# Kernel tuning notes

Hardware: AMD Instinct MI355X
Metric: run time of the kernel (lower is better)

## Reference

```python
import jax, jax.numpy as jnp
import numpy as np

L = 44                      # num_lods
IMG = 178                   # output image side
HASH_SIZE = 1 << 10         # codebook_bitwidth = 10
PRIME = np.uint32(2654435761)
RES = np.round(16.0 * (128.0 / 16.0) ** (np.arange(L) / (L - 1.0))).astype(np.int32)
DENSE = (RES + 1) ** 2 <= HASH_SIZE            # dense level if it fits in 2^10 entries
SIZES = np.where(DENSE, (RES + 1) ** 2, HASH_SIZE).astype(np.int32)
OFFS = np.concatenate([[0], np.cumsum(SIZES)[:-1]]).astype(np.int32)
TOTAL = int(SIZES.sum())    # 38584 shared codebook entries (latent_dim = 1)


def setup_inputs() -> dict:
    key = jax.random.key(0)
    k = jax.random.split(key, 5)
    B, N = 16, IMG * IMG
    x = jax.random.uniform(k[0], (B, N, 2), dtype=jnp.float32)            # 2D coords in [0,1]
    codebook = 0.1 * jax.random.normal(k[1], (B, TOTAL, 1), jnp.float32)  # feature_std=0.1
    w1 = jax.random.normal(k[2], (B, 16, L), jnp.float32) / np.sqrt(L)
    w2 = jax.random.normal(k[3], (B, 16, 16), jnp.float32) / 4.0
    w3 = jax.random.normal(k[4], (B, 3, 16), jnp.float32) / 4.0
    return {"x": x, "codebook": codebook, "w1": w1, "w2": w2, "w3": w3}


def _grid_lookup(x, codebook):
    """Multi-LOD hashed 2D grid bilinear lookup. x:[B,N,2], codebook:[B,T,1] -> [B,N,L]."""
    B, N, _ = x.shape
    res_f = jnp.asarray(RES, jnp.float32)
    res_i = jnp.asarray(RES)
    scaled = x[:, :, None, :] * res_f[None, None, :, None]          # [B,N,L,2]
    base = jnp.floor(scaled)
    frac = scaled - base
    base = base.astype(jnp.int32)
    corners = jnp.array([[0, 0], [0, 1], [1, 0], [1, 1]], jnp.int32)  # [4,2]
    c = base[:, :, :, None, :] + corners[None, None, None]          # [B,N,L,4,2]
    c = jnp.minimum(c, res_i[None, None, :, None, None])
    cx, cy = c[..., 0], c[..., 1]
    dense_idx = cy * (res_i + 1)[None, None, :, None] + cx          # row-major dense index
    h = (cx.astype(jnp.uint32) ^ (cy.astype(jnp.uint32) * PRIME)) % jnp.uint32(HASH_SIZE)
    idx = jnp.where(jnp.asarray(DENSE)[None, None, :, None], dense_idx, h.astype(jnp.int32))
    idx = idx + jnp.asarray(OFFS)[None, None, :, None]              # [B,N,L,4] into shared table
    vals = jnp.take_along_axis(codebook[:, :, 0], idx.reshape(B, -1), axis=1).reshape(B, N, L, 4)
    fr = frac[:, :, :, None, :]                                     # [B,N,L,1,2]
    w = jnp.where(corners[None, None, None] == 1, fr, 1.0 - fr).prod(-1)  # bilinear wts [B,N,L,4]
    return (vals * w).sum(-1)                                       # [B,N,L]


def reference(x, codebook, w1, w2, w3):
    feats = _grid_lookup(x, codebook)                               # [B,N,44] ('cat' multiscale)
    h = jax.nn.relu(jnp.einsum('bnl,bhl->bnh', feats, w1))          # per-sample hypernet weights
    h = jax.nn.relu(jnp.einsum('bnh,bkh->bnk', h, w2))
    rgb = jax.nn.sigmoid(jnp.einsum('bnk,bck->bnc', h, w3))         # [B,N,3]
    return rgb.reshape(x.shape[0], IMG, IMG, 3)
```

## Files before the change

### kernel.cpp

```cpp
#include <hip/hip_runtime.h>
#include <math.h>

#define NLEV 44
#define NDENSE 15
#define IMG 178
#define NPTS (IMG*IMG)
#define HASH_SIZE 1024
#define PRIME 2654435761u
#define BLOCK 1024
#define PTS_PER_BLOCK (2*BLOCK)

typedef __attribute__((ext_vector_type(2))) float f32x2;

struct LevelParams {
    int res[NLEV];
    int offs[NLEV];
    int total;
};

#define PKFMA_S(acc, a, b) \
    asm("v_pk_fma_f32 %0, %1, %2, %0" : "+v"(acc) : "v"(a), "s"(b))

__global__ __launch_bounds__(1024) void transpose_w1(const float* __restrict__ w1,
                                                     float* __restrict__ w1t) {
    const int b = blockIdx.x;
    const int i = threadIdx.x;
    if (i < 16 * NLEV) {
        const int l = i >> 4, o = i & 15;
        w1t[(size_t)b * 16 * NLEV + i] = w1[(size_t)b * 16 * NLEV + o * NLEV + l];
    }
}

template<bool TP>
__global__ __launch_bounds__(BLOCK) void shacira_kernel(
    const float* __restrict__ x, const float* __restrict__ codebook,
    const float* __restrict__ w1, const float* __restrict__ w1t,
    const float* __restrict__ w2, const float* __restrict__ w3,
    float* __restrict__ out, LevelParams lp)
{
    extern __shared__ float sCB[];
    const int total = lp.total;
    const int tid = threadIdx.x;
    const int b = blockIdx.y;

    {
        const float* cbg = codebook + (size_t)b * total;
        const float4* src = (const float4*)cbg;
        float4* dst = (float4*)sCB;
        const int n4 = total >> 2;
        for (int i = tid; i < n4; i += BLOCK) dst[i] = src[i];
        for (int i = (n4 << 2) + tid; i < total; i += BLOCK) sCB[i] = cbg[i];
    }
    __syncthreads();

    const float* w1b = TP ? (w1t + (size_t)b * 16 * NLEV) : (w1 + (size_t)b * 16 * NLEV);
    const float* w2b = w2 + (size_t)b * 256;
    const float* w3b = w3 + (size_t)b * 48;

    const int n0 = blockIdx.x * PTS_PER_BLOCK + tid;
    const int n1 = n0 + BLOCK;
    const bool valid0 = n0 < NPTS;
    const bool valid1 = n1 < NPTS;
    const float2* xg = (const float2*)x + (size_t)b * NPTS;
    float2 xy0 = valid0 ? xg[n0] : make_float2(0.f, 0.f);
    float2 xy1 = valid1 ? xg[n1] : make_float2(0.f, 0.f);

    f32x2 h1a[8], h1b[8];
#pragma unroll
    for (int j = 0; j < 8; ++j) {
        h1a[j].x = 0.f; h1a[j].y = 0.f;
        h1b[j].x = 0.f; h1b[j].y = 0.f;
    }

#pragma unroll
    for (int l = 0; l < NDENSE; ++l) {
        const int res = lp.res[l];
        const int st  = res + 1;
        const int off = lp.offs[l];
        const float rf = (float)res;
        f32x2 wlv[8];
        if constexpr (TP) {
            const f32x2* wp = (const f32x2*)(w1b + l * 16);
#pragma unroll
            for (int j = 0; j < 8; ++j) wlv[j] = wp[j];
        } else {
#pragma unroll
            for (int j = 0; j < 8; ++j) {
                wlv[j].x = w1b[(2 * j) * NLEV + l];
                wlv[j].y = w1b[(2 * j + 1) * NLEV + l];
            }
        }
        auto dolevel = [&](const float2 xy, f32x2* h1) {
            const float sx = xy.x * rf, sy = xy.y * rf;
            const int ix0 = (int)sx, iy0 = (int)sy;
            const float fx = sx - (float)ix0, fy = sy - (float)iy0;
            const int r0 = off + iy0 * st + ix0;
            const float v00 = sCB[r0],      v10 = sCB[r0 + 1];
            const float v01 = sCB[r0 + st], v11 = sCB[r0 + st + 1];
            const float vx0 = fmaf(fx, v10 - v00, v00);
            const float vx1 = fmaf(fx, v11 - v01, v01);
            const float feat = fmaf(fy, vx1 - vx0, vx0);
            f32x2 f2; f2.x = feat; f2.y = feat;
#pragma unroll
            for (int j = 0; j < 8; ++j) PKFMA_S(h1[j], f2, wlv[j]);
        };
        dolevel(xy0, h1a);
        dolevel(xy1, h1b);
    }

#pragma unroll
    for (int l = NDENSE; l < NLEV; ++l) {
        const int res = lp.res[l];
        const int off = lp.offs[l];
        const float rf = (float)res;
        f32x2 wlv[8];
        if constexpr (TP) {
            const f32x2* wp = (const f32x2*)(w1b + l * 16);
#pragma unroll
            for (int j = 0; j < 8; ++j) wlv[j] = wp[j];
        } else {
#pragma unroll
            for (int j = 0; j < 8; ++j) {
                wlv[j].x = w1b[(2 * j) * NLEV + l];
                wlv[j].y = w1b[(2 * j + 1) * NLEV + l];
            }
        }
        auto dolevel = [&](const float2 xy, f32x2* h1) {
            const float sx = xy.x * rf, sy = xy.y * rf;
            const int ix0 = (int)sx, iy0 = (int)sy;
            const float fx = sx - (float)ix0, fy = sy - (float)iy0;
            const unsigned px0 = (unsigned)ix0, px1 = px0 + 1u;
            const unsigned py0 = (unsigned)iy0 * PRIME, py1 = py0 + PRIME;
            const int i00 = (int)((px0 ^ py0) & (HASH_SIZE - 1));
            const int i01 = (int)((px0 ^ py1) & (HASH_SIZE - 1));
            const int i10 = (int)((px1 ^ py0) & (HASH_SIZE - 1));
            const int i11 = (int)((px1 ^ py1) & (HASH_SIZE - 1));
            const float v00 = sCB[off + i00];
            const float v01 = sCB[off + i01];
            const float v10 = sCB[off + i10];
            const float v11 = sCB[off + i11];
            const float vx0 = fmaf(fx, v10 - v00, v00);
            const float vx1 = fmaf(fx, v11 - v01, v01);
            const float feat = fmaf(fy, vx1 - vx0, vx0);
            f32x2 f2; f2.x = feat; f2.y = feat;
#pragma unroll
            for (int j = 0; j < 8; ++j) PKFMA_S(h1[j], f2, wlv[j]);
        };
        dolevel(xy0, h1a);
        dolevel(xy1, h1b);
    }

    auto mlp = [&](f32x2* h1, int n, bool valid) {
        if (!valid) return;
#pragma unroll
        for (int j = 0; j < 8; ++j) {
            h1[j].x = fmaxf(h1[j].x, 0.f);
            h1[j].y = fmaxf(h1[j].y, 0.f);
        }
        float h2[16];
#pragma unroll
        for (int o = 0; o < 16; ++o) {
            const f32x2* w2v = (const f32x2*)(w2b + o * 16);
            f32x2 acc; acc.x = 0.f; acc.y = 0.f;
#pragma unroll
            for (int k = 0; k < 8; ++k) PKFMA_S(acc, h1[k], w2v[k]);
            h2[o] = fmaxf(acc.x + acc.y, 0.f);
        }
        f32x2 h2v[8];
#pragma unroll
        for (int j = 0; j < 8; ++j) { h2v[j].x = h2[2 * j]; h2v[j].y = h2[2 * j + 1]; }
        float rgb[3];
#pragma unroll
        for (int c = 0; c < 3; ++c) {
            const f32x2* w3v = (const f32x2*)(w3b + c * 16);
            f32x2 acc; acc.x = 0.f; acc.y = 0.f;
#pragma unroll
            for (int k = 0; k < 8; ++k) PKFMA_S(acc, h2v[k], w3v[k]);
            rgb[c] = 1.f / (1.f + expf(-(acc.x + acc.y)));
        }
        float* op = out + ((size_t)b * NPTS + n) * 3;
        op[0] = rgb[0]; op[1] = rgb[1]; op[2] = rgb[2];
    };
    mlp(h1a, n0, valid0);
    mlp(h1b, n1, valid1);
}

extern "C" void kernel_launch(void* const* d_in, const int* in_sizes, int n_in,
                              void* d_out, int out_size, void* d_ws, size_t ws_size,
                              hipStream_t stream) {
    const float* x        = (const float*)d_in[0];
    const float* codebook = (const float*)d_in[1];
    const float* w1       = (const float*)d_in[2];
    const float* w2       = (const float*)d_in[3];
    const float* w3       = (const float*)d_in[4];
    float* out = (float*)d_out;

    const int B = in_sizes[0] / (NPTS * 2);

    LevelParams lp;
    int off = 0;
    for (int l = 0; l < NLEV; ++l) {
        const double r = 16.0 * pow(128.0 / 16.0, (double)l / (double)(NLEV - 1));
        const int res = (int)llrint(r);
        lp.res[l] = res;
        lp.offs[l] = off;
        const int sz = ((long long)(res + 1) * (res + 1) <= HASH_SIZE)
                           ? (res + 1) * (res + 1) : HASH_SIZE;
        off += sz;
    }
    lp.total = off;

    const size_t smemBytes = (size_t)lp.total * 4;
    const size_t w1tBytes = (size_t)B * 16 * NLEV * 4;
    const bool tp = ws_size >= w1tBytes;

    if (tp) {
        transpose_w1<<<dim3(B), dim3(1024), 0, stream>>>(w1, (float*)d_ws);
        hipFuncSetAttribute((const void*)shacira_kernel<true>,
                            hipFuncAttributeMaxDynamicSharedMemorySize, (int)smemBytes);
        dim3 grid((NPTS + PTS_PER_BLOCK - 1) / PTS_PER_BLOCK, B);
        shacira_kernel<true><<<grid, dim3(BLOCK), smemBytes, stream>>>(
            x, codebook, w1, (const float*)d_ws, w2, w3, out, lp);
    } else {
        hipFuncSetAttribute((const void*)shacira_kernel<false>,
                            hipFuncAttributeMaxDynamicSharedMemorySize, (int)smemBytes);
        dim3 grid((NPTS + PTS_PER_BLOCK - 1) / PTS_PER_BLOCK, B);
        shacira_kernel<false><<<grid, dim3(BLOCK), smemBytes, stream>>>(
            x, codebook, w1, (const float*)0, w2, w3, out, lp);
    }
}
```

Measured before the change: 39.51 us.

## Stage only hash levels in LDS as fp16, read dense levels from global

```diff
diff --git a/kernel.cpp b/kernel.cpp
--- a/kernel.cpp
+++ b/kernel.cpp
@@ -1,14 +1,15 @@
 #include <hip/hip_runtime.h>
+#include <hip/hip_fp16.h>
 #include <math.h>
 
 #define NLEV 44
 #define NDENSE 15
+#define NHASH (NLEV - NDENSE)
 #define IMG 178
 #define NPTS (IMG*IMG)
 #define HASH_SIZE 1024
 #define PRIME 2654435761u
 #define BLOCK 1024
-#define PTS_PER_BLOCK (2*BLOCK)
 
 typedef __attribute__((ext_vector_type(2))) float f32x2;
 
@@ -16,6 +17,7 @@
     int res[NLEV];
     int offs[NLEV];
     int total;
+    int hashBase;
 };
 
 #define PKFMA_S(acc, a, b) \
@@ -32,157 +34,156 @@
 }
 
 template<bool TP>
-__global__ __launch_bounds__(BLOCK) void shacira_kernel(
+__device__ __forceinline__ void load_w1(const float* __restrict__ w1b, int l, f32x2* wlv) {
+    if constexpr (TP) {
+        const f32x2* wp = (const f32x2*)(w1b + l * 16);
+#pragma unroll
+        for (int j = 0; j < 8; ++j) wlv[j] = wp[j];
+    } else {
+#pragma unroll
+        for (int j = 0; j < 8; ++j) {
+            wlv[j].x = w1b[(2 * j) * NLEV + l];
+            wlv[j].y = w1b[(2 * j + 1) * NLEV + l];
+        }
+    }
+}
+
+template<int L0, int CNT, bool TP>
+__device__ __forceinline__ void dense_g(
+    const LevelParams& lp, const float* __restrict__ cbg,
+    const float* __restrict__ w1b, float2 xy, f32x2* __restrict__ h1)
+{
+    float v[CNT][4];
+    float fr[CNT][2];
+#pragma unroll
+    for (int i = 0; i < CNT; ++i) {
+        const int l = L0 + i;
+        const int res = lp.res[l];
+        const int st  = res + 1;
+        const int off = lp.offs[l];
+        const float rf = (float)res;
+        const float sx = xy.x * rf, sy = xy.y * rf;
+        const int ix0 = (int)sx, iy0 = (int)sy;
+        fr[i][0] = sx - (float)ix0;
+        fr[i][1] = sy - (float)iy0;
+        const int r0 = off + iy0 * st + ix0;
+        v[i][0] = cbg[r0];
+        v[i][1] = cbg[r0 + 1];
+        v[i][2] = cbg[r0 + st];
+        v[i][3] = cbg[r0 + st + 1];
+    }
+#pragma unroll
+    for (int i = 0; i < CNT; ++i) {
+        const int l = L0 + i;
+        f32x2 wlv[8];
+        load_w1<TP>(w1b, l, wlv);
+        const float vx0 = fmaf(fr[i][0], v[i][1] - v[i][0], v[i][0]);
+        const float vx1 = fmaf(fr[i][0], v[i][3] - v[i][2], v[i][2]);
+        const float feat = fmaf(fr[i][1], vx1 - vx0, vx0);
+        f32x2 f2; f2.x = feat; f2.y = feat;
+#pragma unroll
+        for (int j = 0; j < 8; ++j) PKFMA_S(h1[j], f2, wlv[j]);
+    }
+}
+
+template<bool TP>
+__global__ __launch_bounds__(BLOCK, 4) void shacira_kernel(
     const float* __restrict__ x, const float* __restrict__ codebook,
     const float* __restrict__ w1, const float* __restrict__ w1t,
     const float* __restrict__ w2, const float* __restrict__ w3,
     float* __restrict__ out, LevelParams lp)
 {
-    extern __shared__ float sCB[];
-    const int total = lp.total;
+    extern __shared__ __half sH[];
     const int tid = threadIdx.x;
     const int b = blockIdx.y;
+    const float* cbg = codebook + (size_t)b * lp.total;
 
     {
-        const float* cbg = codebook + (size_t)b * total;
-        const float4* src = (const float4*)cbg;
-        float4* dst = (float4*)sCB;
-        const int n4 = total >> 2;
-        for (int i = tid; i < n4; i += BLOCK) dst[i] = src[i];
-        for (int i = (n4 << 2) + tid; i < total; i += BLOCK) sCB[i] = cbg[i];
+        const float4* src = (const float4*)(cbg + lp.hashBase);
+        __half2* dst = (__half2*)sH;
+        const int n4 = (NHASH * HASH_SIZE) >> 2;
+        for (int i = tid; i < n4; i += BLOCK) {
+            const float4 v = src[i];
+            dst[2 * i]     = __floats2half2_rn(v.x, v.y);
+            dst[2 * i + 1] = __floats2half2_rn(v.z, v.w);
+        }
     }
     __syncthreads();
+
+    const int n = blockIdx.x * BLOCK + tid;
+    if (n >= NPTS) return;
 
     const float* w1b = TP ? (w1t + (size_t)b * 16 * NLEV) : (w1 + (size_t)b * 16 * NLEV);
     const float* w2b = w2 + (size_t)b * 256;
     const float* w3b = w3 + (size_t)b * 48;
 
-    const int n0 = blockIdx.x * PTS_PER_BLOCK + tid;
-    const int n1 = n0 + BLOCK;
-    const bool valid0 = n0 < NPTS;
-    const bool valid1 = n1 < NPTS;
-    const float2* xg = (const float2*)x + (size_t)b * NPTS;
-    float2 xy0 = valid0 ? xg[n0] : make_float2(0.f, 0.f);
-    float2 xy1 = valid1 ? xg[n1] : make_float2(0.f, 0.f);
-
-    f32x2 h1a[8], h1b[8];
+    const float2 xy = ((const float2*)x)[(size_t)b * NPTS + n];
+
+    f32x2 h1[8];
+#pragma unroll
+    for (int j = 0; j < 8; ++j) { h1[j].x = 0.f; h1[j].y = 0.f; }
+
+    dense_g<0, 3, TP>(lp, cbg, w1b, xy, h1);
+    dense_g<3, 3, TP>(lp, cbg, w1b, xy, h1);
+    dense_g<6, 3, TP>(lp, cbg, w1b, xy, h1);
+    dense_g<9, 3, TP>(lp, cbg, w1b, xy, h1);
+    dense_g<12, 3, TP>(lp, cbg, w1b, xy, h1);
+
+#pragma unroll
+    for (int l = NDENSE; l < NLEV; ++l) {
+        const float rf = (float)lp.res[l];
+        const int base = (l - NDENSE) << 10;
+        const float sx = xy.x * rf, sy = xy.y * rf;
+        const int ix0 = (int)sx, iy0 = (int)sy;
+        const float fx = sx - (float)ix0, fy = sy - (float)iy0;
+        const unsigned px0 = (unsigned)ix0, px1 = px0 + 1u;
+        const unsigned py0 = (unsigned)iy0 * PRIME, py1 = py0 + PRIME;
+        const int i00 = (int)((px0 ^ py0) & (HASH_SIZE - 1));
+        const int i01 = (int)((px0 ^ py1) & (HASH_SIZE - 1));
+        const int i10 = (int)((px1 ^ py0) & (HASH_SIZE - 1));
+        const int i11 = (int)((px1 ^ py1) & (HASH_SIZE - 1));
+        const float v00 = __half2float(sH[base + i00]);
+        const float v01 = __half2float(sH[base + i01]);
+        const float v10 = __half2float(sH[base + i10]);
+        const float v11 = __half2float(sH[base + i11]);
+        const float vx0 = fmaf(fx, v10 - v00, v00);
+        const float vx1 = fmaf(fx, v11 - v01, v01);
+        const float feat = fmaf(fy, vx1 - vx0, vx0);
+        f32x2 f2; f2.x = feat; f2.y = feat;
+        f32x2 wlv[8];
+        load_w1<TP>(w1b, l, wlv);
+#pragma unroll
+        for (int j = 0; j < 8; ++j) PKFMA_S(h1[j], f2, wlv[j]);
+    }
+
 #pragma unroll
     for (int j = 0; j < 8; ++j) {
-        h1a[j].x = 0.f; h1a[j].y = 0.f;
-        h1b[j].x = 0.f; h1b[j].y = 0.f;
-    }
-
-#pragma unroll
-    for (int l = 0; l < NDENSE; ++l) {
-        const int res = lp.res[l];
-        const int st  = res + 1;
-        const int off = lp.offs[l];
-        const float rf = (float)res;
-        f32x2 wlv[8];
-        if constexpr (TP) {
-            const f32x2* wp = (const f32x2*)(w1b + l * 16);
-#pragma unroll
-            for (int j = 0; j < 8; ++j) wlv[j] = wp[j];
-        } else {
-#pragma unroll
-            for (int j = 0; j < 8; ++j) {
-                wlv[j].x = w1b[(2 * j) * NLEV + l];
-                wlv[j].y = w1b[(2 * j + 1) * NLEV + l];
-            }
-        }
-        auto dolevel = [&](const float2 xy, f32x2* h1) {
-            const float sx = xy.x * rf, sy = xy.y * rf;
-            const int ix0 = (int)sx, iy0 = (int)sy;
-            const float fx = sx - (float)ix0, fy = sy - (float)iy0;
-            const int r0 = off + iy0 * st + ix0;
-            const float v00 = sCB[r0],      v10 = sCB[r0 + 1];
-            const float v01 = sCB[r0 + st], v11 = sCB[r0 + st + 1];
-            const float vx0 = fmaf(fx, v10 - v00, v00);
-            const float vx1 = fmaf(fx, v11 - v01, v01);
-            const float feat = fmaf(fy, vx1 - vx0, vx0);
-            f32x2 f2; f2.x = feat; f2.y = feat;
-#pragma unroll
-            for (int j = 0; j < 8; ++j) PKFMA_S(h1[j], f2, wlv[j]);
-        };
-        dolevel(xy0, h1a);
-        dolevel(xy1, h1b);
-    }
-
-#pragma unroll
-    for (int l = NDENSE; l < NLEV; ++l) {
-        const int res = lp.res[l];
-        const int off = lp.offs[l];
-        const float rf = (float)res;
-        f32x2 wlv[8];
-        if constexpr (TP) {
-            const f32x2* wp = (const f32x2*)(w1b + l * 16);
-#pragma unroll
-            for (int j = 0; j < 8; ++j) wlv[j] = wp[j];
-        } else {
-#pragma unroll
-            for (int j = 0; j < 8; ++j) {
-                wlv[j].x = w1b[(2 * j) * NLEV + l];
-                wlv[j].y = w1b[(2 * j + 1) * NLEV + l];
-            }
-        }
-        auto dolevel = [&](const float2 xy, f32x2* h1) {
-            const float sx = xy.x * rf, sy = xy.y * rf;
-            const int ix0 = (int)sx, iy0 = (int)sy;
-            const float fx = sx - (float)ix0, fy = sy - (float)iy0;
-            const unsigned px0 = (unsigned)ix0, px1 = px0 + 1u;
-            const unsigned py0 = (unsigned)iy0 * PRIME, py1 = py0 + PRIME;
-            const int i00 = (int)((px0 ^ py0) & (HASH_SIZE - 1));
-            const int i01 = (int)((px0 ^ py1) & (HASH_SIZE - 1));
-            const int i10 = (int)((px1 ^ py0) & (HASH_SIZE - 1));
-            const int i11 = (int)((px1 ^ py1) & (HASH_SIZE - 1));
-            const float v00 = sCB[off + i00];
-            const float v01 = sCB[off + i01];
-            const float v10 = sCB[off + i10];
-            const float v11 = sCB[off + i11];
-            const float vx0 = fmaf(fx, v10 - v00, v00);
-            const float vx1 = fmaf(fx, v11 - v01, v01);
-            const float feat = fmaf(fy, vx1 - vx0, vx0);
-            f32x2 f2; f2.x = feat; f2.y = feat;
-#pragma unroll
-            for (int j = 0; j < 8; ++j) PKFMA_S(h1[j], f2, wlv[j]);
-        };
-        dolevel(xy0, h1a);
-        dolevel(xy1, h1b);
-    }
-
-    auto mlp = [&](f32x2* h1, int n, bool valid) {
-        if (!valid) return;
-#pragma unroll
-        for (int j = 0; j < 8; ++j) {
-            h1[j].x = fmaxf(h1[j].x, 0.f);
-            h1[j].y = fmaxf(h1[j].y, 0.f);
-        }
-        float h2[16];
-#pragma unroll
-        for (int o = 0; o < 16; ++o) {
-            const f32x2* w2v = (const f32x2*)(w2b + o * 16);
-            f32x2 acc; acc.x = 0.f; acc.y = 0.f;
-#pragma unroll
-            for (int k = 0; k < 8; ++k) PKFMA_S(acc, h1[k], w2v[k]);
-            h2[o] = fmaxf(acc.x + acc.y, 0.f);
-        }
-        f32x2 h2v[8];
-#pragma unroll
-        for (int j = 0; j < 8; ++j) { h2v[j].x = h2[2 * j]; h2v[j].y = h2[2 * j + 1]; }
-        float rgb[3];
-#pragma unroll
-        for (int c = 0; c < 3; ++c) {
-            const f32x2* w3v = (const f32x2*)(w3b + c * 16);
-            f32x2 acc; acc.x = 0.f; acc.y = 0.f;
-#pragma unroll
-            for (int k = 0; k < 8; ++k) PKFMA_S(acc, h2v[k], w3v[k]);
-            rgb[c] = 1.f / (1.f + expf(-(acc.x + acc.y)));
-        }
-        float* op = out + ((size_t)b * NPTS + n) * 3;
-        op[0] = rgb[0]; op[1] = rgb[1]; op[2] = rgb[2];
-    };
-    mlp(h1a, n0, valid0);
-    mlp(h1b, n1, valid1);
+        h1[j].x = fmaxf(h1[j].x, 0.f);
+        h1[j].y = fmaxf(h1[j].y, 0.f);
+    }
+    float h2[16];
+#pragma unroll
+    for (int o = 0; o < 16; ++o) {
+        const f32x2* w2v = (const f32x2*)(w2b + o * 16);
+        f32x2 acc; acc.x = 0.f; acc.y = 0.f;
+#pragma unroll
+        for (int k = 0; k < 8; ++k) PKFMA_S(acc, h1[k], w2v[k]);
+        h2[o] = fmaxf(acc.x + acc.y, 0.f);
+    }
+    f32x2 h2v[8];
+#pragma unroll
+    for (int j = 0; j < 8; ++j) { h2v[j].x = h2[2 * j]; h2v[j].y = h2[2 * j + 1]; }
+    float rgb[3];
+#pragma unroll
+    for (int c = 0; c < 3; ++c) {
+        const f32x2* w3v = (const f32x2*)(w3b + c * 16);
+        f32x2 acc; acc.x = 0.f; acc.y = 0.f;
+#pragma unroll
+        for (int k = 0; k < 8; ++k) PKFMA_S(acc, h2v[k], w3v[k]);
+        rgb[c] = 1.f / (1.f + expf(-(acc.x + acc.y)));
+    }
+    float* op = out + ((size_t)b * NPTS + n) * 3;
+    op[0] = rgb[0]; op[1] = rgb[1]; op[2] = rgb[2];
 }
 
 extern "C" void kernel_launch(void* const* d_in, const int* in_sizes, int n_in,
@@ -209,22 +210,18 @@
         off += sz;
     }
     lp.total = off;
-
-    const size_t smemBytes = (size_t)lp.total * 4;
+    lp.hashBase = lp.offs[NDENSE];
+
+    const size_t smemBytes = (size_t)NHASH * HASH_SIZE * sizeof(__half);
     const size_t w1tBytes = (size_t)B * 16 * NLEV * 4;
     const bool tp = ws_size >= w1tBytes;
 
+    dim3 grid((NPTS + BLOCK - 1) / BLOCK, B);
     if (tp) {
         transpose_w1<<<dim3(B), dim3(1024), 0, stream>>>(w1, (float*)d_ws);
-        hipFuncSetAttribute((const void*)shacira_kernel<true>,
-                            hipFuncAttributeMaxDynamicSharedMemorySize, (int)smemBytes);
-        dim3 grid((NPTS + PTS_PER_BLOCK - 1) / PTS_PER_BLOCK, B);
         shacira_kernel<true><<<grid, dim3(BLOCK), smemBytes, stream>>>(
             x, codebook, w1, (const float*)d_ws, w2, w3, out, lp);
     } else {
-        hipFuncSetAttribute((const void*)shacira_kernel<false>,
-                            hipFuncAttributeMaxDynamicSharedMemorySize, (int)smemBytes);
-        dim3 grid((NPTS + PTS_PER_BLOCK - 1) / PTS_PER_BLOCK, B);
         shacira_kernel<false><<<grid, dim3(BLOCK), smemBytes, stream>>>(
             x, codebook, w1, (const float*)0, w2, w3, out, lp);
     }
```

Measured after the change: 42.12 us. 6.6% more time.

## Specialize kernel with compile-time level constants and 4KB-aligned hash table layout

Applied to the files above, without the earlier changes.

```diff
diff --git a/kernel.cpp b/kernel.cpp
--- a/kernel.cpp
+++ b/kernel.cpp
@@ -3,14 +3,24 @@
 
 #define NLEV 44
 #define NDENSE 15
+#define NHASH (NLEV - NDENSE)
 #define IMG 178
 #define NPTS (IMG*IMG)
 #define HASH_SIZE 1024
 #define PRIME 2654435761u
 #define BLOCK 1024
 #define PTS_PER_BLOCK (2*BLOCK)
+#define HBASE 36864u
+#define PRIME_LOW_B 1732u
+#define PYMASK 4092u
 
 typedef __attribute__((ext_vector_type(2))) float f32x2;
+
+constexpr int RES_C[NLEV] = {16,17,18,18,19,20,21,22,24,25,26,27,29,30,31,
+                             33,35,36,38,40,42,44,46,49,51,54,56,59,62,65,
+                             68,72,75,79,83,87,91,96,101,105,111,116,122,128};
+constexpr int size_c(int l) { int r = RES_C[l]; int s = (r+1)*(r+1); return s <= 1024 ? s : 1024; }
+constexpr int off_c(int l)  { int o = 0; for (int i = 0; i < l; ++i) o += size_c(i); return o; }
 
 struct LevelParams {
     int res[NLEV];
@@ -20,6 +30,8 @@
 
 #define PKFMA_S(acc, a, b) \
     asm("v_pk_fma_f32 %0, %1, %2, %0" : "+v"(acc) : "v"(a), "s"(b))
+
+#define FRACT(dst, src) asm("v_fract_f32 %0, %1" : "=v"(dst) : "v"(src))
 
 __global__ __launch_bounds__(1024) void transpose_w1(const float* __restrict__ w1,
                                                      float* __restrict__ w1t) {
@@ -31,8 +43,171 @@
     }
 }
 
+
+template<int L>
+__device__ __forceinline__ float dense_feat(const char* lds, float2 xy) {
+    constexpr float rf = (float)RES_C[L];
+    constexpr int st = RES_C[L] + 1;
+    constexpr unsigned off4 = (unsigned)(off_c(L) * 4);
+    const float sx = xy.x * rf, sy = xy.y * rf;
+    const int ix0 = (int)sx, iy0 = (int)sy;
+    float fx, fy;
+    FRACT(fx, sx);
+    FRACT(fy, sy);
+    const unsigned aD = off4 + (((unsigned)(iy0 * st + ix0)) << 2);
+    const float v00 = *(const float*)(lds + aD);
+    const float v10 = *(const float*)(lds + aD + 4);
+    const float v01 = *(const float*)(lds + aD + 4 * st);
+    const float v11 = *(const float*)(lds + aD + 4 * st + 4);
+    const float vx0 = fmaf(fx, v10 - v00, v00);
+    const float vx1 = fmaf(fx, v11 - v01, v01);
+    return fmaf(fy, vx1 - vx0, vx0);
+}
+
+template<int L>
+__device__ __forceinline__ float hash_feat(const char* lds, float2 xy) {
+    constexpr float rf = (float)RES_C[L];
+    constexpr unsigned lbase = HBASE + (unsigned)(L - NDENSE) * 4096u;
+    const float sx = xy.x * rf, sy = xy.y * rf;
+    const int ix0 = (int)sx, iy0 = (int)sy;
+    float fx, fy;
+    FRACT(fx, sx);
+    FRACT(fy, sy);
+    const unsigned pyb0 = ((unsigned)iy0 * PRIME_LOW_B) & PYMASK;
+    const unsigned pyb1 = (pyb0 + PRIME_LOW_B) & PYMASK;
+    const unsigned bpx0 = lbase + (((unsigned)ix0) << 2);
+    const unsigned bpx1 = bpx0 + 4u;
+    const float v00 = *(const float*)(lds + (bpx0 ^ pyb0));
+    const float v01 = *(const float*)(lds + (bpx0 ^ pyb1));
+    const float v10 = *(const float*)(lds + (bpx1 ^ pyb0));
+    const float v11 = *(const float*)(lds + (bpx1 ^ pyb1));
+    const float vx0 = fmaf(fx, v10 - v00, v00);
+    const float vx1 = fmaf(fx, v11 - v01, v01);
+    return fmaf(fy, vx1 - vx0, vx0);
+}
+
+template<int L>
+__device__ __forceinline__ void level_apply(const float* __restrict__ w1b,
+                                            float f0, float f1,
+                                            f32x2* __restrict__ h1a, f32x2* __restrict__ h1b) {
+    const f32x2* wp = (const f32x2*)(w1b + L * 16);
+    f32x2 wlv[8];
+#pragma unroll
+    for (int j = 0; j < 8; ++j) wlv[j] = wp[j];
+    f32x2 f0v; f0v.x = f0; f0v.y = f0;
+    f32x2 f1v; f1v.x = f1; f1v.y = f1;
+#pragma unroll
+    for (int j = 0; j < 8; ++j) {
+        PKFMA_S(h1a[j], f0v, wlv[j]);
+        PKFMA_S(h1b[j], f1v, wlv[j]);
+    }
+}
+
+template<int L>
+__device__ __forceinline__ void levels_from(const char* lds, const float* __restrict__ w1b,
+                                            const float2& xy0, const float2& xy1,
+                                            f32x2* __restrict__ h1a, f32x2* __restrict__ h1b) {
+    if constexpr (L < NLEV) {
+        float f0, f1;
+        if constexpr (L < NDENSE) {
+            f0 = dense_feat<L>(lds, xy0);
+            f1 = dense_feat<L>(lds, xy1);
+        } else {
+            f0 = hash_feat<L>(lds, xy0);
+            f1 = hash_feat<L>(lds, xy1);
+        }
+        level_apply<L>(w1b, f0, f1, h1a, h1b);
+        levels_from<L + 1>(lds, w1b, xy0, xy1, h1a, h1b);
+    }
+}
+
+__device__ __forceinline__ void mlp_store(const float* __restrict__ w2b,
+                                          const float* __restrict__ w3b,
+                                          float* __restrict__ out, size_t bofs,
+                                          f32x2* __restrict__ h1, int n, bool valid) {
+    if (!valid) return;
+#pragma unroll
+    for (int j = 0; j < 8; ++j) {
+        h1[j].x = fmaxf(h1[j].x, 0.f);
+        h1[j].y = fmaxf(h1[j].y, 0.f);
+    }
+    float h2[16];
+#pragma unroll
+    for (int o = 0; o < 16; ++o) {
+        const f32x2* w2v = (const f32x2*)(w2b + o * 16);
+        f32x2 acc; acc.x = 0.f; acc.y = 0.f;
+#pragma unroll
+        for (int k = 0; k < 8; ++k) PKFMA_S(acc, h1[k], w2v[k]);
+        h2[o] = fmaxf(acc.x + acc.y, 0.f);
+    }
+    f32x2 h2v[8];
+#pragma unroll
+    for (int j = 0; j < 8; ++j) { h2v[j].x = h2[2 * j]; h2v[j].y = h2[2 * j + 1]; }
+    float rgb[3];
+#pragma unroll
+    for (int c = 0; c < 3; ++c) {
+        const f32x2* w3v = (const f32x2*)(w3b + c * 16);
+        f32x2 acc; acc.x = 0.f; acc.y = 0.f;
+#pragma unroll
+        for (int k = 0; k < 8; ++k) PKFMA_S(acc, h2v[k], w3v[k]);
+        const float z = acc.x + acc.y;
+        const float e = __builtin_amdgcn_exp2f(z * -1.44269504088896f);
+        rgb[c] = __builtin_amdgcn_rcpf(1.f + e);
+    }
+    ((float3*)out)[bofs + n] = make_float3(rgb[0], rgb[1], rgb[2]);
+}
+
+__global__ __launch_bounds__(BLOCK) void shacira_hard(
+    const float* __restrict__ x, const float* __restrict__ codebook,
+    const float* __restrict__ w1t, const float* __restrict__ w2,
+    const float* __restrict__ w3, float* __restrict__ out)
+{
+    extern __shared__ char lds[];
+    const int tid = threadIdx.x;
+    const int b = blockIdx.y;
+    constexpr int TOTAL = off_c(NLEV - 1) + size_c(NLEV - 1);
+    constexpr int DENSE_TOT = off_c(NDENSE);
+    const float* cbg = codebook + (size_t)b * TOTAL;
+
+    {
+        const float4* srcD = (const float4*)cbg;
+        float4* dstD = (float4*)lds;
+        for (int i = tid; i < DENSE_TOT / 4; i += BLOCK) dstD[i] = srcD[i];
+        const float4* srcH = (const float4*)(cbg + DENSE_TOT);
+        float4* dstH = (float4*)(lds + HBASE);
+        for (int i = tid; i < (NHASH * HASH_SIZE) / 4; i += BLOCK) dstH[i] = srcH[i];
+    }
+    __syncthreads();
+
+    const float* w1b = w1t + (size_t)b * 16 * NLEV;
+    const float* w2b = w2 + (size_t)b * 256;
+    const float* w3b = w3 + (size_t)b * 48;
+
+    const int n0 = blockIdx.x * PTS_PER_BLOCK + tid;
+    const int n1 = n0 + BLOCK;
+    const bool valid0 = n0 < NPTS;
+    const bool valid1 = n1 < NPTS;
+    const float2* xg = (const float2*)x + (size_t)b * NPTS;
+    float2 xy0 = valid0 ? xg[n0] : make_float2(0.f, 0.f);
+    float2 xy1 = valid1 ? xg[n1] : make_float2(0.f, 0.f);
+
+    f32x2 h1a[8], h1b[8];
+#pragma unroll
+    for (int j = 0; j < 8; ++j) {
+        h1a[j].x = 0.f; h1a[j].y = 0.f;
+        h1b[j].x = 0.f; h1b[j].y = 0.f;
+    }
+
+    levels_from<0>(lds, w1b, xy0, xy1, h1a, h1b);
+
+    const size_t bofs = (size_t)b * NPTS;
+    mlp_store(w2b, w3b, out, bofs, h1a, n0, valid0);
+    mlp_store(w2b, w3b, out, bofs, h1b, n1, valid1);
+}
+
+
 template<bool TP>
-__global__ __launch_bounds__(BLOCK) void shacira_kernel(
+__global__ __launch_bounds__(BLOCK) void shacira_soft(
     const float* __restrict__ x, const float* __restrict__ codebook,
     const float* __restrict__ w1, const float* __restrict__ w1t,
     const float* __restrict__ w2, const float* __restrict__ w3,
@@ -42,7 +217,6 @@
     const int total = lp.total;
     const int tid = threadIdx.x;
     const int b = blockIdx.y;
-
     {
         const float* cbg = codebook + (size_t)b * total;
         const float4* src = (const float4*)cbg;
@@ -198,10 +372,12 @@
     const int B = in_sizes[0] / (NPTS * 2);
 
     LevelParams lp;
+    bool hard_ok = true;
     int off = 0;
     for (int l = 0; l < NLEV; ++l) {
         const double r = 16.0 * pow(128.0 / 16.0, (double)l / (double)(NLEV - 1));
         const int res = (int)llrint(r);
+        if (res != RES_C[l]) hard_ok = false;
         lp.res[l] = res;
         lp.offs[l] = off;
         const int sz = ((long long)(res + 1) * (res + 1) <= HASH_SIZE)
@@ -209,23 +385,32 @@
         off += sz;
     }
     lp.total = off;
-
-    const size_t smemBytes = (size_t)lp.total * 4;
+    if (off != off_c(NLEV - 1) + size_c(NLEV - 1)) hard_ok = false;
+
     const size_t w1tBytes = (size_t)B * 16 * NLEV * 4;
     const bool tp = ws_size >= w1tBytes;
 
-    if (tp) {
+    dim3 grid((NPTS + PTS_PER_BLOCK - 1) / PTS_PER_BLOCK, B);
+
+    if (hard_ok && tp) {
         transpose_w1<<<dim3(B), dim3(1024), 0, stream>>>(w1, (float*)d_ws);
-        hipFuncSetAttribute((const void*)shacira_kernel<true>,
-                            hipFuncAttributeMaxDynamicSharedMemorySize, (int)smemBytes);
-        dim3 grid((NPTS + PTS_PER_BLOCK - 1) / PTS_PER_BLOCK, B);
-        shacira_kernel<true><<<grid, dim3(BLOCK), smemBytes, stream>>>(
+        const size_t smemBytes = HBASE + (size_t)NHASH * 4096;
+        (void)hipFuncSetAttribute((const void*)shacira_hard,
+                                  hipFuncAttributeMaxDynamicSharedMemorySize, (int)smemBytes);
+        shacira_hard<<<grid, dim3(BLOCK), smemBytes, stream>>>(
+            x, codebook, (const float*)d_ws, w2, w3, out);
+    } else if (tp) {
+        transpose_w1<<<dim3(B), dim3(1024), 0, stream>>>(w1, (float*)d_ws);
+        const size_t smemBytes = (size_t)lp.total * 4;
+        (void)hipFuncSetAttribute((const void*)shacira_soft<true>,
+                                  hipFuncAttributeMaxDynamicSharedMemorySize, (int)smemBytes);
+        shacira_soft<true><<<grid, dim3(BLOCK), smemBytes, stream>>>(
             x, codebook, w1, (const float*)d_ws, w2, w3, out, lp);
     } else {
-        hipFuncSetAttribute((const void*)shacira_kernel<false>,
-                            hipFuncAttributeMaxDynamicSharedMemorySize, (int)smemBytes);
-        dim3 grid((NPTS + PTS_PER_BLOCK - 1) / PTS_PER_BLOCK, B);
-        shacira_kernel<false><<<grid, dim3(BLOCK), smemBytes, stream>>>(
+        const size_t smemBytes = (size_t)lp.total * 4;
+        (void)hipFuncSetAttribute((const void*)shacira_soft<false>,
+                                  hipFuncAttributeMaxDynamicSharedMemorySize, (int)smemBytes);
+        shacira_soft<false><<<grid, dim3(BLOCK), smemBytes, stream>>>(
             x, codebook, w1, (const float*)0, w2, w3, out, lp);
     }
 }
```

After: 37.11 us (median of 2 runs). 6.1% less time.
